# Performance work log

Measured on AMD Instinct MI355X. Metric: run time of the kernel, lower is better.

## Reference

```python
import jax, jax.numpy as jnp
import numpy as np

N, D, B, E = 3072, 64, 12, 49152


def _gat_conv(x, mask, W, a_src, a_dst, b):
    # PyG GATConv (eval mode): per-edge score = LeakyReLU(a_dst.Wx_i + a_src.Wx_j),
    # softmax over incoming neighbors (mask includes self-loops), concat heads.
    H, d = a_src.shape
    h = (x @ W).reshape(x.shape[0], H, d)                  # [N, H, d]
    es = jnp.einsum('nhd,hd->nh', h, a_src)                # source-side score
    ed = jnp.einsum('nhd,hd->nh', h, a_dst)                # dest-side score
    e = jax.nn.leaky_relu(ed[:, None, :] + es[None, :, :], 0.2)  # [Ndst, Nsrc, H]
    e = jnp.where(mask[:, :, None], e, -jnp.inf)
    alpha = jax.nn.softmax(e, axis=1)                      # softmax over sources
    out = jnp.einsum('ijh,jhd->ihd', alpha, h)
    return out.reshape(x.shape[0], H * d) + b


def _gcn_conv(x, Abool, W, b):
    # PyG GCNConv: add self-loops, symmetric deg^{-1/2} normalization.
    n = x.shape[0]
    Ahat = Abool.astype(x.dtype) + jnp.eye(n, dtype=x.dtype)
    deg = Ahat.sum(1)
    dinv = jnp.where(deg > 0, 1.0 / jnp.sqrt(deg), 0.0)
    return (dinv[:, None] * Ahat * dinv[None, :]) @ (x @ W) + b


def _forward(x, ei, g1_W, g1_as, g1_ad, g1_b, g2_W, g2_as, g2_ad, g2_b,
             gA_W, gA_b, gB_W, gB_b, gC_W, gC_b, c2_W, c2_b, c3_W, c3_b,
             hwA_W, hwA_b, hwB_W, hwB_b, gru_Wih, gru_Whh, gru_bih, gru_bhh,
             tA_W, tA_b, tB_W, tB_b, edge_index, atom_list, res_list):
    n = x.shape[0]
    relu = jax.nn.relu
    I = jnp.eye(n, dtype=bool)
    # A[dst, src] = 1 (PyG messages flow src -> dst); ei only sets to_dense_adj
    # values in the original, which are never used (only adj.shape).
    A = jnp.zeros((n, n), dtype=bool).at[edge_index[1], edge_index[0]].set(True)
    Af = A.astype(x.dtype)
    A2 = (Af @ Af) > 0                      # spspmm(E, E): 2-hop edges
    A3 = (Af @ A2.astype(x.dtype)) > 0      # spspmm(E^2, E): 3-hop edges
    counts = atom_list + res_list
    batch = jnp.repeat(jnp.arange(counts.shape[0]), counts, total_repeat_length=n)

    def gat_block(mask):
        v = jax.nn.elu(_gat_conv(x, mask, g1_W, g1_as, g1_ad, g1_b))
        v = relu(_gat_conv(v, mask, g2_W, g2_as, g2_ad, g2_b))
        v = relu(v @ gA_W + gA_b)
        v = relu(v @ gB_W + gB_b)
        return v @ gC_W + gC_b

    h1 = relu(gat_block(A | I))
    h1 = relu(_gcn_conv(h1, A, c2_W, c2_b))
    h1 = relu(_gcn_conv(h1, A, c3_W, c3_b))          # [N, 4D]
    h2 = relu(gat_block(A2 | I))
    h2 = relu(_gcn_conv(h2, A2, c2_W, c2_b))          # [N, 2D]
    h3 = relu(gat_block(A3 | I))                      # [N, D]
    # HighWay fusion
    bb = h2 @ hwB_W + hwB_b
    aa = h1 @ hwA_W + hwA_b
    z = jax.nn.sigmoid(aa + bb)
    hh = z * bb + (1.0 - z) * aa
    # GRUCell(input=h3, hidden=hh), PyTorch gate order r, z, n
    gx = h3 @ gru_Wih + gru_bih
    gh = hh @ gru_Whh + gru_bhh
    xr, xz, xn = jnp.split(gx, 3, axis=1)
    hr, hz, hn = jnp.split(gh, 3, axis=1)
    r = jax.nn.sigmoid(xr + hr)
    zz = jax.nn.sigmoid(xz + hz)
    nn_ = jnp.tanh(xn + r * hn)
    cc = (1.0 - zz) * nn_ + zz * hh
    vi = jax.ops.segment_max(cc, batch, num_segments=atom_list.shape[0])  # global_max_pool
    vi = relu(vi @ tA_W + tA_b)
    return vi @ tB_W + tB_b


def setup_inputs() -> dict:
    key = jax.random.key(0)
    ks = jax.random.split(key, 40)
    it = iter(range(40))

    def p(shp):
        return jax.random.normal(ks[next(it)], shp, dtype=jnp.float32) * 0.1

    src = jax.random.randint(ks[next(it)], (E,), 0, N)
    dst = jax.random.randint(ks[next(it)], (E,), 0, N)
    dst = jnp.where(dst == src, (dst + 1) % N, dst)   # no self-loops in raw edges
    edge_index = jnp.stack([src, dst])
    inp = {
        'x': jax.random.normal(ks[next(it)], (N, D), dtype=jnp.float32),
        'ei': jax.random.uniform(ks[next(it)], (E,), dtype=jnp.float32),
        'g1_W': p((D, 8 * D)), 'g1_as': p((8, D)), 'g1_ad': p((8, D)), 'g1_b': p((8 * D,)),
        'g2_W': p((8 * D, D)), 'g2_as': p((1, D)), 'g2_ad': p((1, D)), 'g2_b': p((D,)),
        'gA_W': p((D, D)), 'gA_b': p((D,)), 'gB_W': p((D, 128)), 'gB_b': p((128,)),
        'gC_W': p((128, D)), 'gC_b': p((D,)),
        'c2_W': p((D, 2 * D)), 'c2_b': p((2 * D,)), 'c3_W': p((2 * D, 4 * D)), 'c3_b': p((4 * D,)),
        'hwA_W': p((4 * D, D)), 'hwA_b': p((D,)), 'hwB_W': p((2 * D, D)), 'hwB_b': p((D,)),
        'gru_Wih': p((D, 3 * D)), 'gru_Whh': p((D, 3 * D)), 'gru_bih': p((3 * D,)), 'gru_bhh': p((3 * D,)),
        'tA_W': p((D, 128)), 'tA_b': p((128,)), 'tB_W': p((128, 120)), 'tB_b': p((120,)),
        'edge_index': edge_index,
        'atom_list': jnp.full((B,), 156, dtype=jnp.int32),
        'res_list': jnp.full((B,), 100, dtype=jnp.int32),
    }
    return inp


def reference(x, ei, g1_W, g1_as, g1_ad, g1_b, g2_W, g2_as, g2_ad, g2_b,
              gA_W, gA_b, gB_W, gB_b, gC_W, gC_b, c2_W, c2_b, c3_W, c3_b,
              hwA_W, hwA_b, hwB_W, hwB_b, gru_Wih, gru_Whh, gru_bih, gru_bhh,
              tA_W, tA_b, tB_W, tB_b, edge_index, atom_list, res_list):
    return _forward(x, ei, g1_W, g1_as, g1_ad, g1_b, g2_W, g2_as, g2_ad, g2_b,
                    gA_W, gA_b, gB_W, gB_b, gC_W, gC_b, c2_W, c2_b, c3_W, c3_b,
                    hwA_W, hwA_b, hwB_W, hwB_b, gru_Wih, gru_Whh, gru_bih, gru_bhh,
                    tA_W, tA_b, tB_W, tB_b, edge_index, atom_list, res_list)
```

## Files before the change

### kernel.cpp

```cpp
#include <hip/hip_runtime.h>
#include <math.h>

namespace {

constexpr int NN = 3072;
constexpr int NW = 96;
constexpr int NEDGE_C = 49152;
constexpr int NB = 12;

__device__ __forceinline__ float leaky02(float x) { return x > 0.f ? x : 0.2f * x; }
__device__ __forceinline__ float sigm(float x) { return 1.f / (1.f + __expf(-x)); }

template<int ACT> __device__ __forceinline__ float act_apply(float v) {
  if (ACT == 1) return fmaxf(v, 0.f);
  if (ACT == 2) return v > 0.f ? v : (__expf(v) - 1.f);
  return v;
}

__global__ __launch_bounds__(256) void k_scatter(const int* __restrict__ ei,
                                                 unsigned* __restrict__ bits) {
  int e = blockIdx.x * 256 + threadIdx.x;
  if (e < NEDGE_C) {
    int s = ei[e];
    int d = ei[NEDGE_C + e];
    atomicOr(&bits[(size_t)d * NW + (s >> 5)], 1u << (s & 31));
  }
}

__global__ __launch_bounds__(128) void k_bmm(const unsigned* __restrict__ a,
                                             const unsigned* __restrict__ src2,
                                             unsigned* __restrict__ outb) {
  __shared__ unsigned row[NW];
  int d = blockIdx.x;
  int t = threadIdx.x;
  if (t < NW) row[t] = a[(size_t)d * NW + t];
  __syncthreads();
  unsigned acc = 0;
  for (int w = 0; w < NW; ++w) {
    unsigned m = row[w];
    while (m) {
      int b = __ffs(m) - 1; m &= m - 1;
      int k = w * 32 + b;
      if (t < NW) acc |= src2[(size_t)k * NW + t];
    }
  }
  if (t < NW) outb[(size_t)d * NW + t] = acc;
}

__global__ __launch_bounds__(256) void k_dinv(const unsigned* __restrict__ bits,
                                              float* __restrict__ dinv) {
  int i = blockIdx.x * 256 + threadIdx.x;
  if (i < NN) {
    int c = 0;
    for (int w = 0; w < NW; ++w) c += __popc(bits[(size_t)i * NW + w]);
    dinv[i] = 1.0f / sqrtf((float)(c + 1));
  }
}

template<int ACT>
__global__ __launch_bounds__(256) void k_gemm(const float* __restrict__ X,
                                              const float* __restrict__ Wm,
                                              const float* __restrict__ bias,
                                              float* __restrict__ Y,
                                              int K, int Nc) {
  __shared__ float Xt[32][68];
  __shared__ float Wt[32][68];
  int R0 = blockIdx.x * 64, C0 = blockIdx.y * 64;
  int t = threadIdx.x;
  int rg = t >> 4, dg = t & 15;
  float acc[4][4] = {{0.f}};
  for (int k0 = 0; k0 < K; k0 += 32) {
    {
      int r = t >> 2, kq = (t & 3) * 8;
      const float* xp = X + (size_t)(R0 + r) * K + k0 + kq;
      float4 a0 = *(const float4*)xp;
      float4 a1 = *(const float4*)(xp + 4);
      Xt[kq + 0][r] = a0.x; Xt[kq + 1][r] = a0.y; Xt[kq + 2][r] = a0.z; Xt[kq + 3][r] = a0.w;
      Xt[kq + 4][r] = a1.x; Xt[kq + 5][r] = a1.y; Xt[kq + 6][r] = a1.z; Xt[kq + 7][r] = a1.w;
      int kk = t >> 3, cq = (t & 7) * 8;
      const float* wp = Wm + (size_t)(k0 + kk) * Nc + C0 + cq;
      *(float4*)&Wt[kk][cq]     = *(const float4*)wp;
      *(float4*)&Wt[kk][cq + 4] = *(const float4*)(wp + 4);
    }
    __syncthreads();
    #pragma unroll 8
    for (int k = 0; k < 32; ++k) {
      float4 av = *(const float4*)&Xt[k][rg * 4];
      float4 bv = *(const float4*)&Wt[k][dg * 4];
      float ar[4] = {av.x, av.y, av.z, av.w};
      float br[4] = {bv.x, bv.y, bv.z, bv.w};
      #pragma unroll
      for (int ri = 0; ri < 4; ++ri)
        #pragma unroll
        for (int ci = 0; ci < 4; ++ci)
          acc[ri][ci] += ar[ri] * br[ci];
    }
    __syncthreads();
  }
  float bv[4] = {0.f, 0.f, 0.f, 0.f};
  if (bias) {
    bv[0] = bias[C0 + dg * 4 + 0]; bv[1] = bias[C0 + dg * 4 + 1];
    bv[2] = bias[C0 + dg * 4 + 2]; bv[3] = bias[C0 + dg * 4 + 3];
  }
  for (int ri = 0; ri < 4; ++ri) {
    int row = R0 + rg * 4 + ri;
    float4 o;
    float* op = (float*)&o;
    #pragma unroll
    for (int ci = 0; ci < 4; ++ci)
      op[ci] = act_apply<ACT>(acc[ri][ci] + bv[ci]);
    *(float4*)&Y[(size_t)row * Nc + C0 + dg * 4] = o;
  }
}

template<int H>
__global__ __launch_bounds__(64) void k_scores(const float* __restrict__ h,
                                               const float* __restrict__ as,
                                               const float* __restrict__ ad,
                                               float* __restrict__ es,
                                               float* __restrict__ ed) {
  int i = blockIdx.x, lane = threadIdx.x;
  for (int hh = 0; hh < H; ++hh) {
    float v = h[(size_t)i * (H * 64) + hh * 64 + lane];
    float e1 = v * as[hh * 64 + lane];
    float e2 = v * ad[hh * 64 + lane];
    for (int off = 32; off > 0; off >>= 1) {
      e1 += __shfl_down(e1, off);
      e2 += __shfl_down(e2, off);
    }
    if (lane == 0) { es[(size_t)i * H + hh] = e1; ed[(size_t)i * H + hh] = e2; }
  }
}

__global__ __launch_bounds__(256) void k_gmax8(const float* __restrict__ es,
                                               float* __restrict__ gm) {
  __shared__ float sred[256 * 8];
  int t = threadIdx.x;
  float m[8];
  #pragma unroll
  for (int h = 0; h < 8; ++h) m[h] = -3.0e38f;
  for (int j = t; j < NN; j += 256) {
    float4 e0 = *(const float4*)&es[(size_t)j * 8];
    float4 e1 = *(const float4*)&es[(size_t)j * 8 + 4];
    m[0] = fmaxf(m[0], e0.x); m[1] = fmaxf(m[1], e0.y);
    m[2] = fmaxf(m[2], e0.z); m[3] = fmaxf(m[3], e0.w);
    m[4] = fmaxf(m[4], e1.x); m[5] = fmaxf(m[5], e1.y);
    m[6] = fmaxf(m[6], e1.z); m[7] = fmaxf(m[7], e1.w);
  }
  #pragma unroll
  for (int h = 0; h < 8; ++h) sred[t * 8 + h] = m[h];
  __syncthreads();
  for (int s = 128; s > 0; s >>= 1) {
    if (t < s) {
      #pragma unroll
      for (int h = 0; h < 8; ++h)
        sred[t * 8 + h] = fmaxf(sred[t * 8 + h], sred[(t + s) * 8 + h]);
    }
    __syncthreads();
  }
  if (t < 8) gm[t] = sred[t];
}

__global__ __launch_bounds__(256) void k_gmax1b(const float* __restrict__ es,
                                                float* __restrict__ gm) {
  __shared__ float red[256];
  int t = threadIdx.x;
  const float* e = es + (size_t)blockIdx.x * NN;
  float m = -3.0e38f;
  for (int j = t; j < NN; j += 256) m = fmaxf(m, e[j]);
  red[t] = m;
  __syncthreads();
  for (int s = 128; s > 0; s >>= 1) {
    if (t < s) red[t] = fmaxf(red[t], red[t + s]);
    __syncthreads();
  }
  if (t == 0) gm[blockIdx.x] = red[0];
}

__device__ __forceinline__ int enum_bits16(const unsigned* rowb, int p,
                                           unsigned* jlist, int* cnt, int t) {
  if (t < 16) {
    int base = 0;
    for (int k = 0; k < t; ++k) base += __popc(rowb[p * 16 + k]);
    unsigned m = rowb[p * 16 + t];
    int j0 = p * 512 + t * 32;
    while (m) { int b = __ffs(m) - 1; m &= m - 1; jlist[base++] = j0 + b; }
    if (t == 15) *cnt = base;
  }
  __syncthreads();
  return *cnt;
}

template<int ACT>
__global__ __launch_bounds__(256) void k_gat_sparse8(const float* __restrict__ hsrc,
                                                     const float* __restrict__ es,
                                                     const float* __restrict__ ed,
                                                     const float* __restrict__ gm,
                                                     const unsigned* __restrict__ bits,
                                                     const float* __restrict__ bias,
                                                     float* __restrict__ out) {
  __shared__ unsigned rowb[NW];
  __shared__ unsigned jlist[512];
  __shared__ float wl[512 * 8];
  __shared__ int cnt;
  __shared__ float red[256];
  __shared__ float sden[8];
  int i = blockIdx.x, t = threadIdx.x;
  if (t < NW) {
    unsigned wv_ = bits[(size_t)i * NW + t];
    if (t == (i >> 5)) wv_ |= 1u << (i & 31);
    rowb[t] = wv_;
  }
  int wv = t >> 6, lane = t & 63;
  int ha = lane >> 4;
  int hb = 4 + (lane >> 4);
  int ca = lane * 4;
  float4 a0 = {0.f, 0.f, 0.f, 0.f};
  float4 a1 = {0.f, 0.f, 0.f, 0.f};
  int hw = t & 7;
  float edv = ed[(size_t)i * 8 + hw];
  float mh = leaky02(edv + gm[hw]);
  float dloc = 0.f;
  __syncthreads();

  for (int p = 0; p < 6; ++p) {
    __syncthreads();
    int c = enum_bits16(rowb, p, jlist, &cnt, t);
    if (c == 0) continue;
    for (int pidx = t; pidx < c * 8; pidx += 256) {
      int idx = pidx >> 3;
      int j = (int)jlist[idx];
      float s = leaky02(edv + es[(size_t)j * 8 + hw]);
      float w = __expf(s - mh);
      wl[idx * 8 + hw] = w;
      dloc += w;
    }
    __syncthreads();
    int idx = wv;
    for (; idx + 4 < c; idx += 8) {
      int j0 = (int)jlist[idx], j1 = (int)jlist[idx + 4];
      float w0a = wl[idx * 8 + ha],     w0b = wl[idx * 8 + hb];
      float w1a = wl[(idx + 4) * 8 + ha], w1b = wl[(idx + 4) * 8 + hb];
      float4 u0 = *(const float4*)&hsrc[(size_t)j0 * 512 + ca];
      float4 u1 = *(const float4*)&hsrc[(size_t)j0 * 512 + 256 + ca];
      float4 v0 = *(const float4*)&hsrc[(size_t)j1 * 512 + ca];
      float4 v1 = *(const float4*)&hsrc[(size_t)j1 * 512 + 256 + ca];
      a0.x += w0a * u0.x; a0.y += w0a * u0.y; a0.z += w0a * u0.z; a0.w += w0a * u0.w;
      a1.x += w0b * u1.x; a1.y += w0b * u1.y; a1.z += w0b * u1.z; a1.w += w0b * u1.w;
      a0.x += w1a * v0.x; a0.y += w1a * v0.y; a0.z += w1a * v0.z; a0.w += w1a * v0.w;
      a1.x += w1b * v1.x; a1.y += w1b * v1.y; a1.z += w1b * v1.z; a1.w += w1b * v1.w;
    }
    if (idx < c) {
      int j0 = (int)jlist[idx];
      float w0a = wl[idx * 8 + ha], w0b = wl[idx * 8 + hb];
      float4 u0 = *(const float4*)&hsrc[(size_t)j0 * 512 + ca];
      float4 u1 = *(const float4*)&hsrc[(size_t)j0 * 512 + 256 + ca];
      a0.x += w0a * u0.x; a0.y += w0a * u0.y; a0.z += w0a * u0.z; a0.w += w0a * u0.w;
      a1.x += w0b * u1.x; a1.y += w0b * u1.y; a1.z += w0b * u1.z; a1.w += w0b * u1.w;
    }
  }
  __syncthreads();
  red[t] = dloc;
  float* rbuf = wl;
  *(float4*)&rbuf[wv * 512 + ca] = a0;
  *(float4*)&rbuf[wv * 512 + 256 + ca] = a1;
  __syncthreads();
  if (t < 8) {
    float s = 0.f;
    for (int k = t; k < 256; k += 8) s += red[k];
    sden[t] = s;
  }
  __syncthreads();
  int cc0 = 2 * t, h2 = cc0 >> 6;
  float inv = 1.0f / sden[h2];
  float s0 = rbuf[cc0] + rbuf[512 + cc0] + rbuf[1024 + cc0] + rbuf[1536 + cc0];
  float s1 = rbuf[cc0 + 1] + rbuf[512 + cc0 + 1] + rbuf[1024 + cc0 + 1] + rbuf[1536 + cc0 + 1];
  float2 o;
  o.x = act_apply<ACT>(s0 * inv + bias[cc0]);
  o.y = act_apply<ACT>(s1 * inv + bias[cc0 + 1]);
  *(float2*)&out[(size_t)i * 512 + cc0] = o;
}

template<int ACT>
__global__ __launch_bounds__(256) void k_gat_sparse1(const float* __restrict__ hsrc,
                                                     const float* __restrict__ es,
                                                     const float* __restrict__ ed,
                                                     const float* __restrict__ gm,
                                                     const unsigned* __restrict__ bits,
                                                     const float* __restrict__ bias,
                                                     float* __restrict__ out) {
  __shared__ unsigned rowb[NW];
  __shared__ unsigned jlist[512];
  __shared__ float wl[512];
  __shared__ int cnt;
  __shared__ float red[256];
  __shared__ float red2[16 * 64];
  int i = blockIdx.x, t = threadIdx.x;
  if (t < NW) {
    unsigned wv_ = bits[(size_t)i * NW + t];
    if (t == (i >> 5)) wv_ |= 1u << (i & 31);
    rowb[t] = wv_;
  }
  int wv = t >> 6, lane = t & 63;
  int sub = lane >> 4;
  int col4 = (lane & 15) * 4;
  int g = wv * 4 + sub;
  float4 a = {0.f, 0.f, 0.f, 0.f};
  float edv = ed[i];
  float mh = leaky02(edv + gm[0]);
  float dloc = 0.f;
  __syncthreads();

  for (int p = 0; p < 6; ++p) {
    __syncthreads();
    int c = enum_bits16(rowb, p, jlist, &cnt, t);
    if (c == 0) continue;
    for (int idx = t; idx < c; idx += 256) {
      int j = (int)jlist[idx];
      float s = leaky02(edv + es[j]);
      float w = __expf(s - mh);
      wl[idx] = w;
      dloc += w;
    }
    __syncthreads();
    for (int base = 0; base < c; base += 16) {
      int idx = base + g;
      if (idx < c) {
        int j = (int)jlist[idx];
        float w = wl[idx];
        float4 v = *(const float4*)&hsrc[(size_t)j * 64 + col4];
        a.x += w * v.x; a.y += w * v.y; a.z += w * v.z; a.w += w * v.w;
      }
    }
  }
  __syncthreads();
  red[t] = dloc;
  __syncthreads();
  for (int s = 128; s > 0; s >>= 1) {
    if (t < s) red[t] += red[t + s];
    __syncthreads();
  }
  float inv = 1.0f / red[0];
  *(float4*)&red2[g * 64 + col4] = a;
  __syncthreads();
  if (t < 64) {
    float s = 0.f;
    #pragma unroll
    for (int k = 0; k < 16; ++k) s += red2[k * 64 + t];
    out[(size_t)i * 64 + t] = act_apply<ACT>(s * inv + bias[t]);
  }
}

template<int H, int JS>
__global__ __launch_bounds__(256) void k_gat_dense_part(const float* __restrict__ hsrc,
                                                        const float* __restrict__ es,
                                                        const float* __restrict__ ed,
                                                        const float* __restrict__ gm,
                                                        const unsigned* __restrict__ bits,
                                                        float* __restrict__ pacc,
                                                        float* __restrict__ pden) {
  constexpr int CS = H * 64;
  constexpr int TILES = (NN / 32) / JS;
  __shared__ float htile[32][68];
  __shared__ float wl[32][68];
  __shared__ float est[32];
  __shared__ unsigned mword[64];
  __shared__ float edl[64], ml[64];
  __shared__ float sred[4][64];
  int R0 = blockIdx.x * 64;
  int hh = blockIdx.y;
  int z = blockIdx.z;
  int t = threadIdx.x;
  int rg = t >> 4, dg = t & 15;
  int rr = t & 63, jr = t >> 6;
  float acc[4][4] = {{0.f}};
  float spart = 0.f;
  if (t < 64) {
    float e = ed[(size_t)(R0 + t) * H + hh];
    edl[t] = e;
    ml[t] = leaky02(e + gm[hh]);
  }
  __syncthreads();
  for (int tt = 0; tt < TILES; ++tt) {
    int tile = z * TILES + tt;
    int j0 = tile * 32;
    {
      int jj = t >> 3, cq = (t & 7) * 8;
      const float* hp = hsrc + (size_t)(j0 + jj) * CS + hh * 64 + cq;
      *(float4*)&htile[jj][cq]     = *(const float4*)hp;
      *(float4*)&htile[jj][cq + 4] = *(const float4*)(hp + 4);
    }
    if (t < 32) est[t] = es[(size_t)(j0 + t) * H + hh];
    if (t >= 64 && t < 128) mword[t - 64] = bits[(size_t)(R0 + t - 64) * NW + tile];
    __syncthreads();
    {
      unsigned wbits = mword[rr];
      int selfj = (R0 + rr) - j0;
      if (selfj >= 0 && selfj < 32) wbits |= (1u << selfj);
      float edv = edl[rr], mv = ml[rr];
      #pragma unroll
      for (int q = 0; q < 8; ++q) {
        int jj = (q << 2) | jr;
        float w = 0.f;
        if (wbits & (1u << jj)) {
          float s = leaky02(edv + est[jj]);
          w = __expf(s - mv);
        }
        wl[jj][rr] = w;
        spart += w;
      }
    }
    __syncthreads();
    #pragma unroll 8
    for (int jj = 0; jj < 32; ++jj) {
      float4 av = *(const float4*)&wl[jj][rg * 4];
      float4 bv = *(const float4*)&htile[jj][dg * 4];
      float ar[4] = {av.x, av.y, av.z, av.w};
      float br[4] = {bv.x, bv.y, bv.z, bv.w};
      #pragma unroll
      for (int ri = 0; ri < 4; ++ri)
        #pragma unroll
        for (int ci = 0; ci < 4; ++ci)
          acc[ri][ci] += ar[ri] * br[ci];
    }
    __syncthreads();
  }
  sred[jr][rr] = spart;
  __syncthreads();
  if (t < 64)
    pden[((size_t)z * NN + R0 + t) * H + hh] =
        sred[0][t] + sred[1][t] + sred[2][t] + sred[3][t];
  int cbase = hh * 64 + dg * 4;
  for (int ri = 0; ri < 4; ++ri) {
    int r = rg * 4 + ri;
    float4 o;
    o.x = acc[ri][0]; o.y = acc[ri][1]; o.z = acc[ri][2]; o.w = acc[ri][3];
    *(float4*)&pacc[((size_t)z * NN + R0 + r) * CS + cbase] = o;
  }
}

template<int H, int ACT, int JS>
__global__ __launch_bounds__(256) void k_gat_dense_red(const float* __restrict__ pacc,
                                                       const float* __restrict__ pden,
                                                       const float* __restrict__ bias,
                                                       float* __restrict__ out) {
  constexpr int CS = H * 64;
  int idx = blockIdx.x * 256 + threadIdx.x;
  if (idx >= NN * CS) return;
  int row = idx / CS, c = idx - row * CS, hh = c >> 6;
  float a = 0.f, d = 0.f;
  #pragma unroll
  for (int z = 0; z < JS; ++z) a += pacc[((size_t)z * NN + row) * CS + c];
  #pragma unroll
  for (int z = 0; z < JS; ++z) d += pden[((size_t)z * NN + row) * H + hh];
  out[idx] = act_apply<ACT>(a / d + bias[c]);
}

template<int H, int ACT>
__global__ __launch_bounds__(256) void k_gat_dense(const float* __restrict__ hsrc,
                                                   const float* __restrict__ es,
                                                   const float* __restrict__ ed,
                                                   const float* __restrict__ gm,
                                                   const unsigned* __restrict__ bits,
                                                   const float* __restrict__ bias,
                                                   float* __restrict__ out) {
  constexpr int CS = H * 64;
  __shared__ float htile[32][68];
  __shared__ float wl[32][68];
  __shared__ float est[32];
  __shared__ unsigned mword[64];
  __shared__ float edl[64], ml[64];
  __shared__ float sred[4][64];
  int R0 = blockIdx.x * 64;
  int hh = blockIdx.y;
  int t = threadIdx.x;
  int rg = t >> 4, dg = t & 15;
  int rr = t & 63, jr = t >> 6;
  float acc[4][4] = {{0.f}};
  float spart = 0.f;
  if (t < 64) {
    float e = ed[(size_t)(R0 + t) * H + hh];
    edl[t] = e;
    ml[t] = leaky02(e + gm[hh]);
  }
  __syncthreads();
  for (int tile = 0; tile < NN / 32; ++tile) {
    int j0 = tile * 32;
    {
      int jj = t >> 3, cq = (t & 7) * 8;
      const float* hp = hsrc + (size_t)(j0 + jj) * CS + hh * 64 + cq;
      *(float4*)&htile[jj][cq]     = *(const float4*)hp;
      *(float4*)&htile[jj][cq + 4] = *(const float4*)(hp + 4);
    }
    if (t < 32) est[t] = es[(size_t)(j0 + t) * H + hh];
    if (t >= 64 && t < 128) mword[t - 64] = bits[(size_t)(R0 + t - 64) * NW + tile];
    __syncthreads();
    {
      unsigned wbits = mword[rr];
      int selfj = (R0 + rr) - j0;
      if (selfj >= 0 && selfj < 32) wbits |= (1u << selfj);
      float edv = edl[rr], mv = ml[rr];
      #pragma unroll
      for (int q = 0; q < 8; ++q) {
        int jj = (q << 2) | jr;
        float w = 0.f;
        if (wbits & (1u << jj)) {
          float s = leaky02(edv + est[jj]);
          w = __expf(s - mv);
        }
        wl[jj][rr] = w;
        spart += w;
      }
    }
    __syncthreads();
    #pragma unroll 8
    for (int jj = 0; jj < 32; ++jj) {
      float4 av = *(const float4*)&wl[jj][rg * 4];
      float4 bv = *(const float4*)&htile[jj][dg * 4];
      float ar[4] = {av.x, av.y, av.z, av.w};
      float br[4] = {bv.x, bv.y, bv.z, bv.w};
      #pragma unroll
      for (int ri = 0; ri < 4; ++ri)
        #pragma unroll
        for (int ci = 0; ci < 4; ++ci)
          acc[ri][ci] += ar[ri] * br[ci];
    }
    __syncthreads();
  }
  sred[jr][rr] = spart;
  __syncthreads();
  if (t < 64) ml[t] = sred[0][t] + sred[1][t] + sred[2][t] + sred[3][t];
  __syncthreads();
  int cbase = hh * 64 + dg * 4;
  float bv0 = bias[cbase], bv1 = bias[cbase + 1], bv2 = bias[cbase + 2], bv3 = bias[cbase + 3];
  for (int ri = 0; ri < 4; ++ri) {
    int r = rg * 4 + ri;
    float inv = 1.0f / ml[r];
    float4 o;
    o.x = act_apply<ACT>(acc[ri][0] * inv + bv0);
    o.y = act_apply<ACT>(acc[ri][1] * inv + bv1);
    o.z = act_apply<ACT>(acc[ri][2] * inv + bv2);
    o.w = act_apply<ACT>(acc[ri][3] * inv + bv3);
    *(float4*)&out[(size_t)(R0 + r) * CS + cbase] = o;
  }
}

__global__ __launch_bounds__(256) void k_gcn256(const float* __restrict__ xw,
                                                const unsigned* __restrict__ bits,
                                                const float* __restrict__ dinv,
                                                const float* __restrict__ bias,
                                                float* __restrict__ out) {
  __shared__ unsigned rowb[NW];
  __shared__ unsigned jlist[512];
  __shared__ int cnt;
  int i = blockIdx.x, t = threadIdx.x;
  if (t < NW) rowb[t] = bits[(size_t)i * NW + t];
  float acc = 0.f;
  __syncthreads();
  for (int p = 0; p < 6; ++p) {
    __syncthreads();
    int cN = enum_bits16(rowb, p, jlist, &cnt, t);
    for (int idx = 0; idx < cN; ++idx) {
      int j = (int)jlist[idx];
      acc += dinv[j] * xw[(size_t)j * 256 + t];
    }
  }
  float di = dinv[i];
  float v = di * (acc + di * xw[(size_t)i * 256 + t]) + bias[t];
  out[(size_t)i * 256 + t] = fmaxf(v, 0.f);
}

__global__ __launch_bounds__(256) void k_gcn128b(const float* __restrict__ xw,
                                                 const unsigned* __restrict__ b0,
                                                 const unsigned* __restrict__ b1,
                                                 const float* __restrict__ d0,
                                                 const float* __restrict__ d1,
                                                 const float* __restrict__ bias,
                                                 float* __restrict__ outb) {
  __shared__ unsigned rowb[NW];
  __shared__ unsigned jlist[512];
  __shared__ int cnt;
  __shared__ float red[256];
  int blk = blockIdx.x, t = threadIdx.x;
  int br = blk >= NN;
  int i = br ? blk - NN : blk;
  const unsigned* bits = br ? b1 : b0;
  const float* dinv = br ? d1 : d0;
  const float* xb = xw + (size_t)br * NN * 128;
  if (t < NW) rowb[t] = bits[(size_t)i * NW + t];
  int g = t >> 7, c = t & 127;
  float acc = 0.f;
  __syncthreads();
  for (int p = 0; p < 6; ++p) {
    __syncthreads();
    int cN = enum_bits16(rowb, p, jlist, &cnt, t);
    for (int idx = g; idx < cN; idx += 2) {
      int j = (int)jlist[idx];
      acc += dinv[j] * xb[(size_t)j * 128 + c];
    }
  }
  __syncthreads();
  red[t] = acc;
  __syncthreads();
  if (t < 128) {
    acc = red[t] + red[t + 128];
    float di = dinv[i];
    float v = di * (acc + di * xb[(size_t)i * 128 + c]) + bias[c];
    outb[(size_t)blk * 128 + c] = fmaxf(v, 0.f);
  }
}

__global__ __launch_bounds__(256) void k_highway(const float* __restrict__ aa,
                                                 const float* __restrict__ bb,
                                                 float* __restrict__ hh) {
  int idx = blockIdx.x * 256 + threadIdx.x;
  if (idx < NN * 64) {
    float a = aa[idx], b = bb[idx];
    float z = sigm(a + b);
    hh[idx] = z * b + (1.f - z) * a;
  }
}

__global__ __launch_bounds__(256) void k_gru(const float* __restrict__ gx,
                                             const float* __restrict__ gh,
                                             const float* __restrict__ hh,
                                             float* __restrict__ cc) {
  int idx = blockIdx.x * 256 + threadIdx.x;
  if (idx < NN * 64) {
    int i = idx >> 6, d = idx & 63;
    float xr = gx[(size_t)i * 192 + d];
    float xz = gx[(size_t)i * 192 + 64 + d];
    float xn = gx[(size_t)i * 192 + 128 + d];
    float hr = gh[(size_t)i * 192 + d];
    float hz = gh[(size_t)i * 192 + 64 + d];
    float hn = gh[(size_t)i * 192 + 128 + d];
    float r = sigm(xr + hr);
    float z = sigm(xz + hz);
    float n = tanhf(xn + r * hn);
    cc[idx] = (1.f - z) * n + z * hh[idx];
  }
}

__global__ __launch_bounds__(64) void k_pool(const float* __restrict__ cc,
                                             const int* __restrict__ atoms,
                                             const int* __restrict__ resl,
                                             float* __restrict__ vi) {
  int s = blockIdx.x, lane = threadIdx.x;
  int start = 0;
  for (int k = 0; k < s; ++k) start += atoms[k] + resl[k];
  int end = start + atoms[s] + resl[s];
  if (end > NN) end = NN;
  float m = -3.0e38f;
  for (int r = start; r < end; ++r) m = fmaxf(m, cc[(size_t)r * 64 + lane]);
  vi[s * 64 + lane] = m;
}

__global__ __launch_bounds__(256) void k_final(const float* __restrict__ vi,
                                               const float* __restrict__ tAW,
                                               const float* __restrict__ tAb,
                                               const float* __restrict__ tBW,
                                               const float* __restrict__ tBb,
                                               float* __restrict__ out) {
  __shared__ float v[NB * 64];
  __shared__ float t1[NB * 128];
  int t = threadIdx.x;
  for (int idx = t; idx < NB * 64; idx += 256) v[idx] = vi[idx];
  __syncthreads();
  for (int idx = t; idx < NB * 128; idx += 256) {
    int r = idx >> 7, c = idx & 127;
    float a = tAb[c];
    for (int k = 0; k < 64; ++k) a += v[r * 64 + k] * tAW[k * 128 + c];
    t1[idx] = fmaxf(a, 0.f);
  }
  __syncthreads();
  for (int idx = t; idx < NB * 120; idx += 256) {
    int r = idx / 120, c = idx % 120;
    float a = tBb[c];
    for (int k = 0; k < 128; ++k) a += t1[r * 128 + k] * tBW[k * 120 + c];
    out[idx] = a;
  }
}

}

extern "C" void kernel_launch(void* const* d_in, const int* in_sizes, int n_in,
                              void* d_out, int out_size, void* d_ws, size_t ws_size,
                              hipStream_t stream) {
  (void)in_sizes; (void)n_in; (void)out_size;
  const float* x     = (const float*)d_in[0];
  const float* g1_W  = (const float*)d_in[2];
  const float* g1_as = (const float*)d_in[3];
  const float* g1_ad = (const float*)d_in[4];
  const float* g1_b  = (const float*)d_in[5];
  const float* g2_W  = (const float*)d_in[6];
  const float* g2_as = (const float*)d_in[7];
  const float* g2_ad = (const float*)d_in[8];
  const float* g2_b  = (const float*)d_in[9];
  const float* gA_W  = (const float*)d_in[10];
  const float* gA_b  = (const float*)d_in[11];
  const float* gB_W  = (const float*)d_in[12];
  const float* gB_b  = (const float*)d_in[13];
  const float* gC_W  = (const float*)d_in[14];
  const float* gC_b  = (const float*)d_in[15];
  const float* c2_W  = (const float*)d_in[16];
  const float* c2_b  = (const float*)d_in[17];
  const float* c3_W  = (const float*)d_in[18];
  const float* c3_b  = (const float*)d_in[19];
  const float* hwA_W = (const float*)d_in[20];
  const float* hwA_b = (const float*)d_in[21];
  const float* hwB_W = (const float*)d_in[22];
  const float* hwB_b = (const float*)d_in[23];
  const float* gWih  = (const float*)d_in[24];
  const float* gWhh  = (const float*)d_in[25];
  const float* gbih  = (const float*)d_in[26];
  const float* gbhh  = (const float*)d_in[27];
  const float* tA_W  = (const float*)d_in[28];
  const float* tA_b  = (const float*)d_in[29];
  const float* tB_W  = (const float*)d_in[30];
  const float* tB_b  = (const float*)d_in[31];
  const int* edges   = (const int*)d_in[32];
  const int* atoms   = (const int*)d_in[33];
  const int* resl    = (const int*)d_in[34];
  float* out = (float*)d_out;

  unsigned* bitsA  = (unsigned*)d_ws;
  unsigned* bitsA2 = bitsA + (size_t)NN * NW;
  unsigned* bitsA3 = bitsA2 + (size_t)NN * NW;
  float* fp = (float*)(bitsA3 + (size_t)NN * NW);
  float* dinvA  = fp; fp += NN;
  float* dinvA2 = fp; fp += NN;
  float* HB     = fp; fp += (size_t)NN * 512;
  float* ES1    = fp; fp += (size_t)NN * 8;
  float* ED1    = fp; fp += (size_t)NN * 8;
  float* GM1    = fp; fp += 16;
  float* V1ALL  = fp; fp += (size_t)3 * NN * 512;
  float* H2BALL = fp; fp += (size_t)3 * NN * 64;
  float* ES2ALL = fp; fp += (size_t)3 * NN;
  float* ED2ALL = fp; fp += (size_t)3 * NN;
  float* GM2ALL = fp; fp += 16;
  float* V2ALL  = fp; fp += (size_t)3 * NN * 64;
  float* V3ALL  = fp; fp += (size_t)3 * NN * 64;
  float* V4ALL  = fp; fp += (size_t)3 * NN * 128;
  float* V5ALL  = fp; fp += (size_t)3 * NN * 64;
  float* XC2    = fp; fp += (size_t)2 * NN * 128;
  float* TG     = fp; fp += (size_t)2 * NN * 128;
  float* XC3    = fp; fp += (size_t)NN * 256;
  float* H1F    = fp; fp += (size_t)NN * 256;
  float* AAb    = fp; fp += (size_t)NN * 64;
  float* BBb    = fp; fp += (size_t)NN * 64;
  float* HHb    = fp; fp += (size_t)NN * 64;
  float* VI     = fp; fp += NB * 64;
  float* GX = V1ALL;
  float* GH = V1ALL + (size_t)NN * 192;
  float* CC = V1ALL + (size_t)NN * 384;
  size_t used = (size_t)((char*)fp - (char*)d_ws);
  size_t pden_f = (size_t)8 * NN * 8;
  size_t need8 = used + ((size_t)8 * NN * 512 + pden_f) * 4;
  size_t need4 = used + ((size_t)4 * NN * 512 + pden_f) * 4;
  int mode = (ws_size >= need8) ? 2 : ((ws_size >= need4) ? 1 : 0);
  float* PACC = fp;
  float* PDEN = PACC + ((mode == 2) ? (size_t)8 * NN * 512 : (size_t)4 * NN * 512);

  float* H3F = V5ALL + (size_t)2 * NN * 64;
  float* H2F = TG + (size_t)NN * 128;

  hipMemsetAsync(bitsA, 0, (size_t)NN * NW * sizeof(unsigned), stream);
  k_scatter<<<(NEDGE_C + 255) / 256, 256, 0, stream>>>(edges, bitsA);
  k_bmm<<<NN, 128, 0, stream>>>(bitsA, bitsA, bitsA2);
  k_bmm<<<NN, 128, 0, stream>>>(bitsA, bitsA2, bitsA3);
  k_dinv<<<NN / 256, 256, 0, stream>>>(bitsA, dinvA);
  k_dinv<<<NN / 256, 256, 0, stream>>>(bitsA2, dinvA2);

  k_gemm<0><<<dim3(48, 8), 256, 0, stream>>>(x, g1_W, nullptr, HB, 64, 512);
  k_scores<8><<<NN, 64, 0, stream>>>(HB, g1_as, g1_ad, ES1, ED1);
  k_gmax8<<<1, 256, 0, stream>>>(ES1, GM1);

  k_gat_sparse8<2><<<NN, 256, 0, stream>>>(HB, ES1, ED1, GM1, bitsA, g1_b, V1ALL);
  k_gat_sparse8<2><<<NN, 256, 0, stream>>>(HB, ES1, ED1, GM1, bitsA2, g1_b, V1ALL + (size_t)NN * 512);
  if (mode == 2) {
    k_gat_dense_part<8, 8><<<dim3(48, 8, 8), 256, 0, stream>>>(HB, ES1, ED1, GM1, bitsA3, PACC, PDEN);
    k_gat_dense_red<8, 2, 8><<<NN * 512 / 256, 256, 0, stream>>>(PACC, PDEN, g1_b, V1ALL + (size_t)2 * NN * 512);
  } else if (mode == 1) {
    k_gat_dense_part<8, 4><<<dim3(48, 8, 4), 256, 0, stream>>>(HB, ES1, ED1, GM1, bitsA3, PACC, PDEN);
    k_gat_dense_red<8, 2, 4><<<NN * 512 / 256, 256, 0, stream>>>(PACC, PDEN, g1_b, V1ALL + (size_t)2 * NN * 512);
  } else {
    k_gat_dense<8, 2><<<dim3(48, 8), 256, 0, stream>>>(HB, ES1, ED1, GM1, bitsA3, g1_b, V1ALL + (size_t)2 * NN * 512);
  }

  k_gemm<0><<<dim3(144, 1), 256, 0, stream>>>(V1ALL, g2_W, nullptr, H2BALL, 512, 64);
  k_scores<1><<<3 * NN, 64, 0, stream>>>(H2BALL, g2_as, g2_ad, ES2ALL, ED2ALL);
  k_gmax1b<<<3, 256, 0, stream>>>(ES2ALL, GM2ALL);

  k_gat_sparse1<1><<<NN, 256, 0, stream>>>(H2BALL, ES2ALL, ED2ALL, GM2ALL, bitsA, g2_b, V2ALL);
  k_gat_sparse1<1><<<NN, 256, 0, stream>>>(H2BALL + (size_t)NN * 64, ES2ALL + NN, ED2ALL + NN,
                                           GM2ALL + 1, bitsA2, g2_b, V2ALL + (size_t)NN * 64);
  if (mode >= 1) {
    k_gat_dense_part<1, 16><<<dim3(48, 1, 16), 256, 0, stream>>>(
        H2BALL + (size_t)2 * NN * 64, ES2ALL + 2 * NN, ED2ALL + 2 * NN, GM2ALL + 2, bitsA3, PACC, PDEN);
    k_gat_dense_red<1, 1, 16><<<NN * 64 / 256, 256, 0, stream>>>(PACC, PDEN, g2_b, V2ALL + (size_t)2 * NN * 64);
  } else {
    k_gat_dense<1, 1><<<dim3(48, 1), 256, 0, stream>>>(
        H2BALL + (size_t)2 * NN * 64, ES2ALL + 2 * NN, ED2ALL + 2 * NN, GM2ALL + 2, bitsA3, g2_b,
        V2ALL + (size_t)2 * NN * 64);
  }

  k_gemm<1><<<dim3(144, 1), 256, 0, stream>>>(V2ALL, gA_W, gA_b, V3ALL, 64, 64);
  k_gemm<1><<<dim3(144, 2), 256, 0, stream>>>(V3ALL, gB_W, gB_b, V4ALL, 64, 128);
  k_gemm<1><<<dim3(144, 1), 256, 0, stream>>>(V4ALL, gC_W, gC_b, V5ALL, 128, 64);

  k_gemm<0><<<dim3(96, 2), 256, 0, stream>>>(V5ALL, c2_W, nullptr, XC2, 64, 128);
  k_gcn128b<<<2 * NN, 256, 0, stream>>>(XC2, bitsA, bitsA2, dinvA, dinvA2, c2_b, TG);
  k_gemm<0><<<dim3(48, 4), 256, 0, stream>>>(TG, c3_W, nullptr, XC3, 128, 256);
  k_gcn256<<<NN, 256, 0, stream>>>(XC3, bitsA, dinvA, c3_b, H1F);

  k_gemm<0><<<dim3(48, 1), 256, 0, stream>>>(H1F, hwA_W, hwA_b, AAb, 256, 64);
  k_gemm<0><<<dim3(48, 1), 256, 0, stream>>>(H2F, hwB_W, hwB_b, BBb, 128, 64);
  k_highway<<<NN * 64 / 256, 256, 0, stream>>>(AAb, BBb, HHb);
  k_gemm<0><<<dim3(48, 3), 256, 0, stream>>>(H3F, gWih, gbih, GX, 64, 192);
  k_gemm<0><<<dim3(48, 3), 256, 0, stream>>>(HHb, gWhh, gbhh, GH, 64, 192);
  k_gru<<<NN * 64 / 256, 256, 0, stream>>>(GX, GH, HHb, CC);
  k_pool<<<NB, 64, 0, stream>>>(CC, atoms, resl, VI);
  k_final<<<1, 256, 0, stream>>>(VI, tA_W, tA_b, tB_W, tB_b, out);
}
```

Baseline: 684.1 us.

## Use split-bf16 MFMA for dense 3-hop GAT aggregation with transposed H

Replaces the FP32 outer-product loop in the dense 3-hop GAT aggregation with bf16 MFMA 16x16x32 instructions. Each operand is split into a high and a low bf16 part, and three MFMAs are used to keep close to fp32 accuracy. A new kernel pre-transposes and splits the source features into column-major bf16 buffers, and the workspace plan drops the 8-way split mode in favour of a fixed 4-way split. This trades an extra transpose kernel and packing work for matrix-core throughput, and the split approximation may differ slightly in accuracy.

```diff
diff --git a/kernel.cpp b/kernel.cpp
--- a/kernel.cpp
+++ b/kernel.cpp
@@ -8,8 +8,28 @@
 constexpr int NEDGE_C = 49152;
 constexpr int NB = 12;
 
+using short8v = __attribute__((ext_vector_type(8))) short;
+using f32x4v  = __attribute__((ext_vector_type(4))) float;
+typedef unsigned short ushort_t;
+
 __device__ __forceinline__ float leaky02(float x) { return x > 0.f ? x : 0.2f * x; }
 __device__ __forceinline__ float sigm(float x) { return 1.f / (1.f + __expf(-x)); }
+
+__device__ __forceinline__ ushort_t f2bf(float x) {
+  unsigned u = __float_as_uint(x);
+  return (ushort_t)((u + 0x7fffu + ((u >> 16) & 1u)) >> 16);
+}
+__device__ __forceinline__ float bf2f(ushort_t b) {
+  return __uint_as_float(((unsigned)b) << 16);
+}
+__device__ __forceinline__ unsigned pack_h(float a, float b) {
+  return (unsigned)f2bf(a) | ((unsigned)f2bf(b) << 16);
+}
+__device__ __forceinline__ unsigned pack_l(float a, float b) {
+  float ra = a - bf2f(f2bf(a));
+  float rb = b - bf2f(f2bf(b));
+  return (unsigned)f2bf(ra) | ((unsigned)f2bf(rb) << 16);
+}
 
 template<int ACT> __device__ __forceinline__ float act_apply(float v) {
   if (ACT == 1) return fmaxf(v, 0.f);
@@ -351,91 +371,136 @@
   }
 }
 
+__global__ __launch_bounds__(256) void k_split_h(const float* __restrict__ hb, int CS,
+                                                 ushort_t* __restrict__ hhT,
+                                                 ushort_t* __restrict__ hlT) {
+  __shared__ float T[64][65];
+  int j0 = blockIdx.x * 64, hh = blockIdx.y;
+  int t = threadIdx.x;
+  int cb = (t & 15) * 4, jrow = t >> 4;
+  #pragma unroll
+  for (int p = 0; p < 4; ++p) {
+    int j = jrow + 16 * p;
+    float4 v = *(const float4*)&hb[(size_t)(j0 + j) * CS + hh * 64 + cb];
+    T[j][cb] = v.x; T[j][cb + 1] = v.y; T[j][cb + 2] = v.z; T[j][cb + 3] = v.w;
+  }
+  __syncthreads();
+  int c = t >> 2, jq = (t & 3) * 16;
+  float x[16];
+  #pragma unroll
+  for (int k = 0; k < 16; ++k) x[k] = T[jq + k][c];
+  size_t base = ((size_t)hh * 64 + c) * NN + j0 + jq;
+  uint4 u;
+  u.x = pack_h(x[0], x[1]);  u.y = pack_h(x[2], x[3]);
+  u.z = pack_h(x[4], x[5]);  u.w = pack_h(x[6], x[7]);
+  *(uint4*)&hhT[base] = u;
+  u.x = pack_h(x[8], x[9]);  u.y = pack_h(x[10], x[11]);
+  u.z = pack_h(x[12], x[13]); u.w = pack_h(x[14], x[15]);
+  *(uint4*)&hhT[base + 8] = u;
+  u.x = pack_l(x[0], x[1]);  u.y = pack_l(x[2], x[3]);
+  u.z = pack_l(x[4], x[5]);  u.w = pack_l(x[6], x[7]);
+  *(uint4*)&hlT[base] = u;
+  u.x = pack_l(x[8], x[9]);  u.y = pack_l(x[10], x[11]);
+  u.z = pack_l(x[12], x[13]); u.w = pack_l(x[14], x[15]);
+  *(uint4*)&hlT[base + 8] = u;
+}
+
 template<int H, int JS>
-__global__ __launch_bounds__(256) void k_gat_dense_part(const float* __restrict__ hsrc,
-                                                        const float* __restrict__ es,
-                                                        const float* __restrict__ ed,
-                                                        const float* __restrict__ gm,
-                                                        const unsigned* __restrict__ bits,
-                                                        float* __restrict__ pacc,
-                                                        float* __restrict__ pden) {
+__global__ __launch_bounds__(256) void k_gat_dense_mfma(
+    const ushort_t* __restrict__ hhT,
+    const ushort_t* __restrict__ hlT,
+    const float* __restrict__ es,
+    const float* __restrict__ ed,
+    const float* __restrict__ gm,
+    const unsigned* __restrict__ bits,
+    float* __restrict__ pacc,
+    float* __restrict__ pden) {
   constexpr int CS = H * 64;
   constexpr int TILES = (NN / 32) / JS;
-  __shared__ float htile[32][68];
-  __shared__ float wl[32][68];
+  constexpr int LW = 40;
+  __shared__ ushort_t WhS[64 * LW], WlS[64 * LW];
+  __shared__ ushort_t BhS[64 * LW], BlS[64 * LW];
   __shared__ float est[32];
   __shared__ unsigned mword[64];
   __shared__ float edl[64], ml[64];
   __shared__ float sred[4][64];
-  int R0 = blockIdx.x * 64;
-  int hh = blockIdx.y;
-  int z = blockIdx.z;
+  int R0 = blockIdx.x * 64, hh = blockIdx.y, z = blockIdx.z;
   int t = threadIdx.x;
-  int rg = t >> 4, dg = t & 15;
   int rr = t & 63, jr = t >> 6;
-  float acc[4][4] = {{0.f}};
+  int wid = t >> 6, lane = t & 63;
+  int arow = lane & 15, kg = lane >> 4;
+  int sc = t >> 2, sjo = (t & 3) * 8;
+  const ushort_t* hhp = hhT + ((size_t)hh * 64 + sc) * NN + sjo;
+  const ushort_t* hlp = hlT + ((size_t)hh * 64 + sc) * NN + sjo;
+  f32x4v acc[4];
+  #pragma unroll
+  for (int nf = 0; nf < 4; ++nf) acc[nf] = (f32x4v){0.f, 0.f, 0.f, 0.f};
   float spart = 0.f;
   if (t < 64) {
     float e = ed[(size_t)(R0 + t) * H + hh];
     edl[t] = e;
     ml[t] = leaky02(e + gm[hh]);
   }
-  __syncthreads();
+  int aoff = (wid * 16 + arow) * LW + kg * 8;
+
   for (int tt = 0; tt < TILES; ++tt) {
-    int tile = z * TILES + tt;
-    int j0 = tile * 32;
-    {
-      int jj = t >> 3, cq = (t & 7) * 8;
-      const float* hp = hsrc + (size_t)(j0 + jj) * CS + hh * 64 + cq;
-      *(float4*)&htile[jj][cq]     = *(const float4*)hp;
-      *(float4*)&htile[jj][cq + 4] = *(const float4*)(hp + 4);
-    }
+    int tile = z * TILES + tt, j0 = tile * 32;
+    __syncthreads();
+    uint4 rbh = *(const uint4*)(hhp + j0);
+    uint4 rbl = *(const uint4*)(hlp + j0);
     if (t < 32) est[t] = es[(size_t)(j0 + t) * H + hh];
     if (t >= 64 && t < 128) mword[t - 64] = bits[(size_t)(R0 + t - 64) * NW + tile];
     __syncthreads();
+    *(uint4*)&BhS[sc * LW + sjo] = rbh;
+    *(uint4*)&BlS[sc * LW + sjo] = rbl;
     {
       unsigned wbits = mword[rr];
       int selfj = (R0 + rr) - j0;
       if (selfj >= 0 && selfj < 32) wbits |= (1u << selfj);
       float edv = edl[rr], mv = ml[rr];
+      float w[8];
       #pragma unroll
       for (int q = 0; q < 8; ++q) {
-        int jj = (q << 2) | jr;
-        float w = 0.f;
-        if (wbits & (1u << jj)) {
-          float s = leaky02(edv + est[jj]);
-          w = __expf(s - mv);
-        }
-        wl[jj][rr] = w;
-        spart += w;
+        int jj = jr * 8 + q;
+        float v = 0.f;
+        if (wbits & (1u << jj)) v = __expf(leaky02(edv + est[jj]) - mv);
+        w[q] = v;
+        spart += v;
       }
-    }
-    __syncthreads();
-    #pragma unroll 8
-    for (int jj = 0; jj < 32; ++jj) {
-      float4 av = *(const float4*)&wl[jj][rg * 4];
-      float4 bv = *(const float4*)&htile[jj][dg * 4];
-      float ar[4] = {av.x, av.y, av.z, av.w};
-      float br[4] = {bv.x, bv.y, bv.z, bv.w};
-      #pragma unroll
-      for (int ri = 0; ri < 4; ++ri)
-        #pragma unroll
-        for (int ci = 0; ci < 4; ++ci)
-          acc[ri][ci] += ar[ri] * br[ci];
-    }
-    __syncthreads();
-  }
+      uint4 uh, ul;
+      uh.x = pack_h(w[0], w[1]); uh.y = pack_h(w[2], w[3]);
+      uh.z = pack_h(w[4], w[5]); uh.w = pack_h(w[6], w[7]);
+      ul.x = pack_l(w[0], w[1]); ul.y = pack_l(w[2], w[3]);
+      ul.z = pack_l(w[4], w[5]); ul.w = pack_l(w[6], w[7]);
+      *(uint4*)&WhS[rr * LW + jr * 8] = uh;
+      *(uint4*)&WlS[rr * LW + jr * 8] = ul;
+    }
+    __syncthreads();
+    short8v Ah = *(const short8v*)&WhS[aoff];
+    short8v Al = *(const short8v*)&WlS[aoff];
+    #pragma unroll
+    for (int nf = 0; nf < 4; ++nf) {
+      short8v bh = *(const short8v*)&BhS[(nf * 16 + arow) * LW + kg * 8];
+      short8v bl = *(const short8v*)&BlS[(nf * 16 + arow) * LW + kg * 8];
+      acc[nf] = __builtin_amdgcn_mfma_f32_16x16x32_bf16(Ah, bh, acc[nf], 0, 0, 0);
+      acc[nf] = __builtin_amdgcn_mfma_f32_16x16x32_bf16(Ah, bl, acc[nf], 0, 0, 0);
+      acc[nf] = __builtin_amdgcn_mfma_f32_16x16x32_bf16(Al, bh, acc[nf], 0, 0, 0);
+    }
+  }
+  __syncthreads();
   sred[jr][rr] = spart;
   __syncthreads();
   if (t < 64)
     pden[((size_t)z * NN + R0 + t) * H + hh] =
         sred[0][t] + sred[1][t] + sred[2][t] + sred[3][t];
-  int cbase = hh * 64 + dg * 4;
-  for (int ri = 0; ri < 4; ++ri) {
-    int r = rg * 4 + ri;
-    float4 o;
-    o.x = acc[ri][0]; o.y = acc[ri][1]; o.z = acc[ri][2]; o.w = acc[ri][3];
-    *(float4*)&pacc[((size_t)z * NN + R0 + r) * CS + cbase] = o;
+  #pragma unroll
+  for (int nf = 0; nf < 4; ++nf) {
+    #pragma unroll
+    for (int r = 0; r < 4; ++r) {
+      int row = R0 + wid * 16 + kg * 4 + r;
+      int c = hh * 64 + nf * 16 + arow;
+      pacc[((size_t)z * NN + row) * CS + c] = acc[nf][r];
+    }
   }
 }
 
@@ -753,13 +818,14 @@
   float* GX = V1ALL;
   float* GH = V1ALL + (size_t)NN * 192;
   float* CC = V1ALL + (size_t)NN * 384;
-  size_t used = (size_t)((char*)fp - (char*)d_ws);
-  size_t pden_f = (size_t)8 * NN * 8;
-  size_t need8 = used + ((size_t)8 * NN * 512 + pden_f) * 4;
-  size_t need4 = used + ((size_t)4 * NN * 512 + pden_f) * 4;
-  int mode = (ws_size >= need8) ? 2 : ((ws_size >= need4) ? 1 : 0);
-  float* PACC = fp;
-  float* PDEN = PACC + ((mode == 2) ? (size_t)8 * NN * 512 : (size_t)4 * NN * 512);
+  char* cp = (char*)fp;
+  ushort_t* HhT8 = (ushort_t*)cp; cp += (size_t)8 * 64 * NN * 2;
+  ushort_t* HlT8 = (ushort_t*)cp; cp += (size_t)8 * 64 * NN * 2;
+  ushort_t* HhT1 = (ushort_t*)cp; cp += (size_t)64 * NN * 2;
+  ushort_t* HlT1 = (ushort_t*)cp; cp += (size_t)64 * NN * 2;
+  float* PACC = (float*)cp; cp += (size_t)4 * NN * 512 * 4;
+  float* PDEN = (float*)cp; cp += (size_t)16 * NN * 8 * 4;
+  int mode = ((size_t)(cp - (char*)d_ws) <= ws_size) ? 1 : 0;
 
   float* H3F = V5ALL + (size_t)2 * NN * 64;
   float* H2F = TG + (size_t)NN * 128;
@@ -777,11 +843,9 @@
 
   k_gat_sparse8<2><<<NN, 256, 0, stream>>>(HB, ES1, ED1, GM1, bitsA, g1_b, V1ALL);
   k_gat_sparse8<2><<<NN, 256, 0, stream>>>(HB, ES1, ED1, GM1, bitsA2, g1_b, V1ALL + (size_t)NN * 512);
-  if (mode == 2) {
-    k_gat_dense_part<8, 8><<<dim3(48, 8, 8), 256, 0, stream>>>(HB, ES1, ED1, GM1, bitsA3, PACC, PDEN);
-    k_gat_dense_red<8, 2, 8><<<NN * 512 / 256, 256, 0, stream>>>(PACC, PDEN, g1_b, V1ALL + (size_t)2 * NN * 512);
-  } else if (mode == 1) {
-    k_gat_dense_part<8, 4><<<dim3(48, 8, 4), 256, 0, stream>>>(HB, ES1, ED1, GM1, bitsA3, PACC, PDEN);
+  if (mode) {
+    k_split_h<<<dim3(48, 8), 256, 0, stream>>>(HB, 512, HhT8, HlT8);
+    k_gat_dense_mfma<8, 4><<<dim3(48, 8, 4), 256, 0, stream>>>(HhT8, HlT8, ES1, ED1, GM1, bitsA3, PACC, PDEN);
     k_gat_dense_red<8, 2, 4><<<NN * 512 / 256, 256, 0, stream>>>(PACC, PDEN, g1_b, V1ALL + (size_t)2 * NN * 512);
   } else {
     k_gat_dense<8, 2><<<dim3(48, 8), 256, 0, stream>>>(HB, ES1, ED1, GM1, bitsA3, g1_b, V1ALL + (size_t)2 * NN * 512);
@@ -794,9 +858,10 @@
   k_gat_sparse1<1><<<NN, 256, 0, stream>>>(H2BALL, ES2ALL, ED2ALL, GM2ALL, bitsA, g2_b, V2ALL);
   k_gat_sparse1<1><<<NN, 256, 0, stream>>>(H2BALL + (size_t)NN * 64, ES2ALL + NN, ED2ALL + NN,
                                            GM2ALL + 1, bitsA2, g2_b, V2ALL + (size_t)NN * 64);
-  if (mode >= 1) {
-    k_gat_dense_part<1, 16><<<dim3(48, 1, 16), 256, 0, stream>>>(
-        H2BALL + (size_t)2 * NN * 64, ES2ALL + 2 * NN, ED2ALL + 2 * NN, GM2ALL + 2, bitsA3, PACC, PDEN);
+  if (mode) {
+    k_split_h<<<dim3(48, 1), 256, 0, stream>>>(H2BALL + (size_t)2 * NN * 64, 64, HhT1, HlT1);
+    k_gat_dense_mfma<1, 16><<<dim3(48, 1, 16), 256, 0, stream>>>(
+        HhT1, HlT1, ES2ALL + 2 * NN, ED2ALL + 2 * NN, GM2ALL + 2, bitsA3, PACC, PDEN);
     k_gat_dense_red<1, 1, 16><<<NN * 64 / 256, 256, 0, stream>>>(PACC, PDEN, g2_b, V2ALL + (size_t)2 * NN * 64);
   } else {
     k_gat_dense<1, 1><<<dim3(48, 1), 256, 0, stream>>>(
```

After: 607.0 us. 1.13x faster.
